# Performance work log

Hardware: AMD Instinct MI355X
Metric: run time of the kernel (lower is better)

The kernel has to match this reference:

```python
import jax, jax.numpy as jnp
from jax import lax
import numpy as np

K, O, I, KS = 4, 128, 128, 5
B, H, W = 32, 64, 64
PAD = 2


def setup_inputs() -> dict:
    key = jax.random.key(0)
    ks = jax.random.split(key, 7)
    x = jax.random.normal(ks[0], (B, I, H, W), dtype=jnp.float32)
    weight = jax.random.normal(ks[1], (K, O, I, KS, KS), dtype=jnp.float32)  # matches torch.randn init
    bias = jax.random.normal(ks[2], (K, O), dtype=jnp.float32)
    # attention: 1x1 convs on a (B,C,1,1) pooled tensor == dense layers
    a1_w = jax.random.normal(ks[3], (I, I), dtype=jnp.float32) * (1.0 / np.sqrt(I))
    a1_b = jax.random.normal(ks[4], (I,), dtype=jnp.float32) * 0.01
    a2_w = jax.random.normal(ks[5], (K, I), dtype=jnp.float32) * (1.0 / np.sqrt(I))
    a2_b = jax.random.normal(ks[6], (K,), dtype=jnp.float32) * 0.01
    return {"x": x, "weight": weight, "bias": bias,
            "a1_w": a1_w, "a1_b": a1_b, "a2_w": a2_w, "a2_b": a2_b}


def reference(x, weight, bias, a1_w, a1_b, a2_w, a2_b):
    Bn = x.shape[0]
    Kn, On, In, kh, kw = weight.shape
    # attention branch: global avg pool -> 1x1 conv -> relu -> 1x1 conv -> softmax over K
    pooled = jnp.mean(x, axis=(2, 3))                       # (B, C)
    h = jax.nn.relu(pooled @ a1_w.T + a1_b)                 # (B, C)
    attn = jax.nn.softmax(h @ a2_w.T + a2_b, axis=1)        # (B, K)
    # K parallel convs fused as one conv with K*O output channels (same math)
    w = weight.reshape(Kn * On, In, kh, kw)
    out = lax.conv_general_dilated(
        x, w, window_strides=(1, 1), padding=((PAD, PAD), (PAD, PAD)),
        dimension_numbers=("NCHW", "OIHW", "NCHW"))        # (B, K*O, H, W)
    Ho, Wo = out.shape[2], out.shape[3]
    out = out.reshape(Bn, Kn, On, Ho, Wo) + bias[None, :, :, None, None]
    # per-sample softmax-weighted combination over the K branches
    return jnp.einsum("bk,bkohw->bohw", attn, out)
```

## Files before the change

### kernel.cpp

```cpp
#include <hip/hip_runtime.h>
#include <stdint.h>

#define BATCH 32
#define ICH 128
#define OCH 128
#define KBR 4
#define HH 64
#define WW 64
#define TAPS 25
#define XROWS 8
#define XCOLS 68
#define XCP 40
#define WROWP 40

typedef __bf16 bf16x8 __attribute__((ext_vector_type(8)));
typedef float f32x4 __attribute__((ext_vector_type(4)));

static __device__ __forceinline__ ushort f2bf(float f) {
    union { float f; uint32_t u; } v; v.f = f;
    uint32_t u = v.u;
    uint32_t r = (u + 0x7FFFu + ((u >> 16) & 1u)) >> 16;
    return (ushort)r;
}
static __device__ __forceinline__ float bf2f(ushort s) {
    union { uint32_t u; float f; } v; v.u = ((uint32_t)s) << 16;
    return v.f;
}

__global__ __launch_bounds__(256) void k_prep(const float* __restrict__ x,
                                              ushort* __restrict__ xT,
                                              float* __restrict__ partial) {
    int blk = blockIdx.x;
    int b = blk >> 6, y = blk & 63;
    __shared__ __align__(16) ushort tile[64][130];
    const float* src = x + ((size_t)b * ICH) * (HH * WW) + (size_t)y * WW;
    int tid = threadIdx.x;
#pragma unroll
    for (int j = 0; j < 32; ++j) {
        int e = tid + 256 * j;
        int i = e >> 6, xc = e & 63;
        float v = src[(size_t)i * (HH * WW) + xc];
        tile[xc][i] = f2bf(v);
    }
    __syncthreads();
    uint* dst = (uint*)(xT + (((size_t)b * HH + y) * WW) * ICH);
#pragma unroll
    for (int j = 0; j < 16; ++j) {
        int p = tid + 256 * j;
        int xc = p >> 6, ih = (p & 63) * 2;
        uint v = (uint)tile[xc][ih] | ((uint)tile[xc][ih + 1] << 16);
        dst[p] = v;
    }
    if (tid < 128) {
        float s = 0.f;
        for (int xc = 0; xc < 64; ++xc) s += bf2f(tile[xc][tid]);
        partial[((size_t)b * HH + y) * ICH + tid] = s;
    }
}

__global__ __launch_bounds__(128) void k_attn(const float* __restrict__ partial,
                                              const float* __restrict__ a1_w,
                                              const float* __restrict__ a1_b,
                                              const float* __restrict__ a2_w,
                                              const float* __restrict__ a2_b,
                                              const float* __restrict__ bias,
                                              float* __restrict__ attn,
                                              float* __restrict__ bias_eff) {
    int b = blockIdx.x;
    int t = threadIdx.x;
    __shared__ float pl[128], hh[128], lg[4], at[4];
    {
        float s = 0.f;
        const float* p = partial + (size_t)b * 64 * 128 + t;
        for (int y = 0; y < 64; ++y) s += p[y * 128];
        pl[t] = s * (1.f / 4096.f);
    }
    __syncthreads();
    {
        float a = a1_b[t];
        const float* w1 = a1_w + t * 128;
        for (int i = 0; i < 128; ++i) a += pl[i] * w1[i];
        hh[t] = a > 0.f ? a : 0.f;
    }
    __syncthreads();
    if (t < 4) {
        float l = a2_b[t];
        const float* w2 = a2_w + t * 128;
        for (int i = 0; i < 128; ++i) l += hh[i] * w2[i];
        lg[t] = l;
    }
    __syncthreads();
    if (t == 0) {
        float m = fmaxf(fmaxf(lg[0], lg[1]), fmaxf(lg[2], lg[3]));
        float e0 = expf(lg[0] - m), e1 = expf(lg[1] - m);
        float e2 = expf(lg[2] - m), e3 = expf(lg[3] - m);
        float inv = 1.f / (e0 + e1 + e2 + e3);
        at[0] = e0 * inv; at[1] = e1 * inv; at[2] = e2 * inv; at[3] = e3 * inv;
        attn[b * 4 + 0] = at[0]; attn[b * 4 + 1] = at[1];
        attn[b * 4 + 2] = at[2]; attn[b * 4 + 3] = at[3];
    }
    __syncthreads();
    bias_eff[b * 128 + t] = at[0] * bias[0 * 128 + t] + at[1] * bias[1 * 128 + t] +
                            at[2] * bias[2 * 128 + t] + at[3] * bias[3 * 128 + t];
}

__global__ __launch_bounds__(256) void k_wcomb(const float* __restrict__ weight,
                                               const float* __restrict__ attn,
                                               ushort* __restrict__ Weff) {
    int blk = blockIdx.x;
    int b = blk >> 7, o = blk & 127;
    float a0 = attn[b * 4 + 0], a1 = attn[b * 4 + 1];
    float a2 = attn[b * 4 + 2], a3 = attn[b * 4 + 3];
    __shared__ float wt[3200];
    const float* w = weight + (size_t)o * 3200;
    for (int e = threadIdx.x; e < 3200; e += 256) {
        wt[e] = a0 * w[e] + a1 * w[409600 + e] + a2 * w[819200 + e] + a3 * w[1228800 + e];
    }
    __syncthreads();
    ushort* dst = Weff + ((size_t)(b * 128 + o)) * 3200;
    for (int f = threadIdx.x; f < 3200; f += 256) {
        int t = f >> 7, i = f & 127;
        dst[f] = f2bf(wt[i * 25 + t]);
    }
}

__global__ __launch_bounds__(512) void k_conv(const ushort* __restrict__ xT,
                                              const ushort* __restrict__ Weff,
                                              const float* __restrict__ bias_eff,
                                              float* __restrict__ out) {
    __shared__ __align__(16) ushort lx[XROWS * XCOLS * XCP];
    __shared__ __align__(16) ushort lw[128 * WROWP];

    int blk = blockIdx.x;
    int b = blk >> 4, rg = blk & 15;
    int y0 = rg * 4;
    int tid = threadIdx.x;
    int lane = tid & 63, wid = tid >> 6;
    int wm = wid >> 2, wn = wid & 3;
    int row16 = lane & 15, kg = lane >> 4;

    f32x4 acc[4][4];
    f32x4 zero = {0.f, 0.f, 0.f, 0.f};
#pragma unroll
    for (int m = 0; m < 4; ++m)
#pragma unroll
        for (int n = 0; n < 4; ++n) acc[m][n] = zero;

    const ushort* xb = xT + ((size_t)b * HH * WW) * ICH;
    const ushort* wb = Weff + ((size_t)b * OCH) * 3200;

    for (int ic = 0; ic < 128; ic += 32) {
        __syncthreads();
        for (int q = tid; q < XROWS * XCOLS * 4; q += 512) {
            int s = q / (XCOLS * 4);
            int rem = q - s * (XCOLS * 4);
            int c = rem >> 2, part = rem & 3;
            int gy = y0 - 2 + s, gx = c - 2;
            uint4 val = make_uint4(0u, 0u, 0u, 0u);
            if (gy >= 0 && gy < 64 && gx >= 0 && gx < 64) {
                val = *(const uint4*)(xb + ((size_t)(gy * 64 + gx)) * ICH + ic + part * 8);
            }
            *(uint4*)(&lx[(s * XCOLS + c) * XCP + part * 8]) = val;
        }
        for (int t = 0; t < TAPS; ++t) {
            __syncthreads();
            {
                int o = tid >> 2, part = tid & 3;
                uint4 wv = *(const uint4*)(wb + ((size_t)o * 25 + t) * 128 + ic + part * 8);
                *(uint4*)(&lw[o * WROWP + part * 8]) = wv;
            }
            __syncthreads();
            int kh = t / 5, kw = t - kh * 5;
            bf16x8 af[4], bfr[4];
#pragma unroll
            for (int m = 0; m < 4; ++m) {
                int o = wm * 64 + m * 16 + row16;
                af[m] = *(const bf16x8*)(&lw[o * WROWP + kg * 8]);
            }
#pragma unroll
            for (int n = 0; n < 4; ++n) {
                int px = wn * 64 + n * 16 + row16;
                int yl = px >> 6, xc = px & 63;
                int s = yl + kh, cc = xc + kw;
                bfr[n] = *(const bf16x8*)(&lx[(s * XCOLS + cc) * XCP + kg * 8]);
            }
#pragma unroll
            for (int m = 0; m < 4; ++m)
#pragma unroll
                for (int n = 0; n < 4; ++n)
                    acc[m][n] = __builtin_amdgcn_mfma_f32_16x16x32_bf16(af[m], bfr[n], acc[m][n], 0, 0, 0);
        }
    }

    float* ob = out + ((size_t)b * OCH) * (HH * WW);
#pragma unroll
    for (int m = 0; m < 4; ++m) {
#pragma unroll
        for (int r = 0; r < 4; ++r) {
            int o = wm * 64 + m * 16 + kg * 4 + r;
            float be = bias_eff[b * 128 + o];
#pragma unroll
            for (int n = 0; n < 4; ++n) {
                int px = wn * 64 + n * 16 + row16;
                int y = y0 + (px >> 6), xc = px & 63;
                ob[((size_t)o * 64 + y) * 64 + xc] = acc[m][n][r] + be;
            }
        }
    }
}

extern "C" void kernel_launch(void* const* d_in, const int* in_sizes, int n_in,
                              void* d_out, int out_size, void* d_ws, size_t ws_size,
                              hipStream_t stream) {
    const float* x      = (const float*)d_in[0];
    const float* weight = (const float*)d_in[1];
    const float* bias   = (const float*)d_in[2];
    const float* a1_w   = (const float*)d_in[3];
    const float* a1_b   = (const float*)d_in[4];
    const float* a2_w   = (const float*)d_in[5];
    const float* a2_b   = (const float*)d_in[6];
    float* out = (float*)d_out;

    const size_t WS_REQUIRED = 60834304;
    if (ws_size < WS_REQUIRED) return;

    char* ws = (char*)d_ws;
    ushort* xT       = (ushort*)(ws);
    ushort* Weff     = (ushort*)(ws + 33554432);
    float*  partial  = (float*)(ws + 59768832);
    float*  attn     = (float*)(ws + 60817408);
    float*  bias_eff = (float*)(ws + 60817920);

    k_prep<<<dim3(BATCH * HH), dim3(256), 0, stream>>>(x, xT, partial);
    k_attn<<<dim3(BATCH), dim3(128), 0, stream>>>(partial, a1_w, a1_b, a2_w, a2_b, bias,
                                                  attn, bias_eff);
    k_wcomb<<<dim3(BATCH * OCH), dim3(256), 0, stream>>>(weight, attn, Weff);
    k_conv<<<dim3(BATCH * 16), dim3(512), 0, stream>>>(xT, Weff, bias_eff, out);
}
```

Baseline: 255.8 us.

## Double-buffer conv weight tiles, remap blocks across XCDs, vectorize prep loads

The conv main loop now double-buffers the per-tap weight tile in LDS. The next tap's weights are loaded into registers before the MFMA work and written to the other buffer afterwards, which cuts the two barriers per tap down to one. Block indices are remapped so each XCD handles contiguous batches, aiming for better L2 reuse of each batch's weights and input. The prep kernel also reads x with float4 loads instead of scalar loads. The cost is a larger LDS footprint and more register pressure.

```diff
diff --git a/kernel.cpp b/kernel.cpp
--- a/kernel.cpp
+++ b/kernel.cpp
@@ -36,11 +36,14 @@
     const float* src = x + ((size_t)b * ICH) * (HH * WW) + (size_t)y * WW;
     int tid = threadIdx.x;
 #pragma unroll
-    for (int j = 0; j < 32; ++j) {
-        int e = tid + 256 * j;
+    for (int j = 0; j < 8; ++j) {
+        int e = (tid + 256 * j) * 4;
         int i = e >> 6, xc = e & 63;
-        float v = src[(size_t)i * (HH * WW) + xc];
-        tile[xc][i] = f2bf(v);
+        float4 v = *(const float4*)(src + (size_t)i * (HH * WW) + xc);
+        tile[xc + 0][i] = f2bf(v.x);
+        tile[xc + 1][i] = f2bf(v.y);
+        tile[xc + 2][i] = f2bf(v.z);
+        tile[xc + 3][i] = f2bf(v.w);
     }
     __syncthreads();
     uint* dst = (uint*)(xT + (((size_t)b * HH + y) * WW) * ICH);
@@ -129,10 +132,12 @@
                                               const float* __restrict__ bias_eff,
                                               float* __restrict__ out) {
     __shared__ __align__(16) ushort lx[XROWS * XCOLS * XCP];
-    __shared__ __align__(16) ushort lw[128 * WROWP];
+    __shared__ __align__(16) ushort lw[2][128 * WROWP];
 
     int blk = blockIdx.x;
-    int b = blk >> 4, rg = blk & 15;
+    int xcd = blk & 7, slot = blk >> 3;
+    int b = xcd * 4 + (slot >> 4);
+    int rg = slot & 15;
     int y0 = rg * 4;
     int tid = threadIdx.x;
     int lane = tid & 63, wid = tid >> 6;
@@ -149,33 +154,41 @@
     const ushort* xb = xT + ((size_t)b * HH * WW) * ICH;
     const ushort* wb = Weff + ((size_t)b * OCH) * 3200;
 
-    for (int ic = 0; ic < 128; ic += 32) {
-        __syncthreads();
+    int wo = tid >> 2, wpart = tid & 3;
+
+    {
         for (int q = tid; q < XROWS * XCOLS * 4; q += 512) {
             int s = q / (XCOLS * 4);
             int rem = q - s * (XCOLS * 4);
             int c = rem >> 2, part = rem & 3;
             int gy = y0 - 2 + s, gx = c - 2;
             uint4 val = make_uint4(0u, 0u, 0u, 0u);
-            if (gy >= 0 && gy < 64 && gx >= 0 && gx < 64) {
-                val = *(const uint4*)(xb + ((size_t)(gy * 64 + gx)) * ICH + ic + part * 8);
-            }
+            if (gy >= 0 && gy < 64 && gx >= 0 && gx < 64)
+                val = *(const uint4*)(xb + ((size_t)(gy * 64 + gx)) * ICH + 0 + part * 8);
             *(uint4*)(&lx[(s * XCOLS + c) * XCP + part * 8]) = val;
         }
-        for (int t = 0; t < TAPS; ++t) {
-            __syncthreads();
-            {
-                int o = tid >> 2, part = tid & 3;
-                uint4 wv = *(const uint4*)(wb + ((size_t)o * 25 + t) * 128 + ic + part * 8);
-                *(uint4*)(&lw[o * WROWP + part * 8]) = wv;
-            }
-            __syncthreads();
+        uint4 wv = *(const uint4*)(wb + ((size_t)wo * 25 + 0) * 128 + 0 + wpart * 8);
+        *(uint4*)(&lw[0][wo * WROWP + wpart * 8]) = wv;
+    }
+    __syncthreads();
+
+    for (int g = 0; g < 100; ++g) {
+        int buf = g & 1;
+        int t = g % 25;
+        uint4 wv;
+        bool have_next = (g + 1 < 100);
+        if (have_next) {
+            int gn = g + 1;
+            int icn = (gn / 25) * 32, tn = gn % 25;
+            wv = *(const uint4*)(wb + ((size_t)wo * 25 + tn) * 128 + icn + wpart * 8);
+        }
+        {
             int kh = t / 5, kw = t - kh * 5;
             bf16x8 af[4], bfr[4];
 #pragma unroll
             for (int m = 0; m < 4; ++m) {
                 int o = wm * 64 + m * 16 + row16;
-                af[m] = *(const bf16x8*)(&lw[o * WROWP + kg * 8]);
+                af[m] = *(const bf16x8*)(&lw[buf][o * WROWP + kg * 8]);
             }
 #pragma unroll
             for (int n = 0; n < 4; ++n) {
@@ -189,6 +202,28 @@
 #pragma unroll
                 for (int n = 0; n < 4; ++n)
                     acc[m][n] = __builtin_amdgcn_mfma_f32_16x16x32_bf16(af[m], bfr[n], acc[m][n], 0, 0, 0);
+        }
+        if (have_next) {
+            *(uint4*)(&lw[buf ^ 1][wo * WROWP + wpart * 8]) = wv;
+        }
+        if (t == 24) {
+            __syncthreads();
+            if (g < 99) {
+                int icn = ((g + 1) / 25) * 32;
+                for (int q = tid; q < XROWS * XCOLS * 4; q += 512) {
+                    int s = q / (XCOLS * 4);
+                    int rem = q - s * (XCOLS * 4);
+                    int c = rem >> 2, part = rem & 3;
+                    int gy = y0 - 2 + s, gx = c - 2;
+                    uint4 val = make_uint4(0u, 0u, 0u, 0u);
+                    if (gy >= 0 && gy < 64 && gx >= 0 && gx < 64)
+                        val = *(const uint4*)(xb + ((size_t)(gy * 64 + gx)) * ICH + icn + part * 8);
+                    *(uint4*)(&lx[(s * XCOLS + c) * XCP + part * 8]) = val;
+                }
+            }
+            __syncthreads();
+        } else {
+            __syncthreads();
         }
     }
 
```

New measurement: 241.2 us. -5.7%, faster.
